# Optimization experiments

Measured on AMD Instinct MI355X. Metric: run time of the kernel, lower is better.

Reference implementation:

```python
import jax, jax.numpy as jnp
import numpy as np

# StyleGAN3 constants
FILTER_SIZE = 6
LRELU_UPSAMPLE = 2
SAMPLING_RATE = 128
CUTOFF = 64
HALF_WIDTH = 32
SLOPE = 0.01

UP = LRELU_UPSAMPLE                       # tmp_resize_factor = 2
NUM_TAPS = FILTER_SIZE * UP               # 12
_pad_total = -1 + (NUM_TAPS - 1) * 2      # 21
PAD_LO = (_pad_total + UP) // 2           # 11
PAD_HI = _pad_total - PAD_LO              # 10


def design_lowpass_filter(numtaps, cutoff, width, fs):
    """numpy re-implementation of scipy.signal.firwin(numtaps, cutoff, width=width, fs=fs)."""
    nyq = 0.5 * fs
    # kaiser_atten / kaiser_beta (scipy formulas)
    wn = width / nyq
    a = 2.285 * (numtaps - 1) * np.pi * wn + 7.95
    if a > 50:
        beta = 0.1102 * (a - 8.7)
    elif a > 21:
        beta = 0.5842 * (a - 21) ** 0.4 + 0.07886 * (a - 21)
    else:
        beta = 0.0
    alpha = 0.5 * (numtaps - 1)
    m = np.arange(numtaps) - alpha
    c = cutoff / nyq
    h = c * np.sinc(c * m) * np.kaiser(numtaps, beta)
    h = h / h.sum()  # scale so DC gain == 1 (firwin scale=True for lowpass)
    return jnp.asarray(h, dtype=jnp.float32)


def setup_inputs() -> dict:
    key = jax.random.key(0)
    x = jax.random.normal(key, (8, 128, 128, 128), dtype=jnp.float32)
    f = design_lowpass_filter(NUM_TAPS, CUTOFF, HALF_WIDTH * 2, SAMPLING_RATE * UP)
    return {"x": x, "f": f}


def _filtered_lrelu(x, f):
    """upfirdn2d(up=2, pad, gain=4) -> leaky_relu (gain=1) -> upfirdn2d(down=2)."""
    N, C, H, W = x.shape
    xr = x.reshape(N * C, 1, H, W)            # depthwise via batch folding
    fk = f[::-1].astype(x.dtype)              # conv (not xcorr), matches torch upfirdn2d flip
    dn = ("NCHW", "OIHW", "NCHW")
    g = jnp.asarray(UP, x.dtype)              # up**2 total gain, split over the 2 separable passes
    # --- upsample by 2 (zero insertion via lhs_dilation) + separable FIR ---
    # lhs_dilation yields length 2H-1 (no trailing zero) -> fold the trailing zero into pad_hi (+up-1)
    kv = (fk * g).reshape(1, 1, -1, 1)
    y = jax.lax.conv_general_dilated(xr, kv, (1, 1), ((PAD_LO, PAD_HI + UP - 1), (0, 0)),
                                     lhs_dilation=(UP, UP), dimension_numbers=dn)
    kh = (fk * g).reshape(1, 1, 1, -1)
    y = jax.lax.conv_general_dilated(y, kh, (1, 1), ((0, 0), (PAD_LO, PAD_HI + UP - 1)),
                                     dimension_numbers=dn)
    # --- leaky ReLU (overall gain = 1.0, clamp = None) ---
    y = jnp.where(y >= 0, y, y * jnp.asarray(SLOPE, y.dtype))
    # --- separable FIR + downsample by 2 (stride) ---
    y = jax.lax.conv_general_dilated(y, fk.reshape(1, 1, -1, 1), (UP, 1), ((0, 0), (0, 0)),
                                     dimension_numbers=dn)
    y = jax.lax.conv_general_dilated(y, fk.reshape(1, 1, 1, -1), (1, UP), ((0, 0), (0, 0)),
                                     dimension_numbers=dn)
    Ho, Wo = y.shape[-2], y.shape[-1]         # == H, W
    return y.reshape(N, C, Ho, Wo)


def reference(x, f):
    return _filtered_lrelu(x, f)
```

## Files before the change

### kernel.cpp

```cpp
#include <hip/hip_runtime.h>


#define TAPS 12
#define VS2 0
#define VSS2 44
#define ZS 1628
#define ZSS 44
#define XS 1628
#define XSS 44
#define WS 0
#define WSS 44
#define LDS_DW 4884

typedef _Float16 half_t;
typedef half_t h2 __attribute__((ext_vector_type(2)));
typedef __fp16 g2 __attribute__((ext_vector_type(2)));
typedef float f2 __attribute__((ext_vector_type(2)));

__device__ __forceinline__ h2 u2h(unsigned u){ h2 r; __builtin_memcpy(&r, &u, 4); return r; }
__device__ __forceinline__ g2 u2g(unsigned u){ g2 r; __builtin_memcpy(&r, &u, 4); return r; }
__device__ __forceinline__ unsigned h2du(h2 h){ unsigned u; __builtin_memcpy(&u, &h, 4); return u; }
__device__ __forceinline__ unsigned pkrtz_u(float lo, float hi){
    g2 p = __builtin_amdgcn_cvt_pkrtz(lo, hi);
    unsigned u; __builtin_memcpy(&u, &p, 4); return u;
}
__device__ __forceinline__ h2 h2s(float v){ h2 r; r.x = (half_t)v; r.y = r.x; return r; }
__device__ __forceinline__ unsigned pack2(half_t a, half_t b){ h2 t; t.x=a; t.y=b; return h2du(t); }

__global__ __launch_bounds__(256) void flrelu_fused(
    const float* __restrict__ x, const float* __restrict__ f, float* __restrict__ out)
{
    __shared__ float smem[LDS_DW];
    unsigned* smemu = reinterpret_cast<unsigned*>(smem);

    const int tid = threadIdx.x;
    const int nc  = blockIdx.y;
    const int ho0 = (blockIdx.x >> 2) * 32;
    const int wo0 = (blockIdx.x & 3) * 32;

    float fkU[TAPS];
#pragma unroll
    for (int t = 0; t < TAPS; ++t) fkU[t] = 2.0f * f[TAPS - 1 - t];

    const float* xin = x + (size_t)nc * (128 * 128);

    if (tid < 252) {
        int c = tid % 42, r0 = tid / 42;
        int gc = wo0 - 5 + c;
        bool gcok = (unsigned)gc < 128u;
        int gcc = gc < 0 ? 0 : (gc > 127 ? 127 : gc);
#pragma unroll
        for (int k = 0; k < 7; ++k) {
            int r = r0 + 6 * k;
            int gr = ho0 - 5 + r;
            int grc = gr < 0 ? 0 : (gr > 127 ? 127 : gr);
            float v = xin[grc * 128 + gcc];
            bool ok = gcok && ((unsigned)gr < 128u);
            smem[XS + r * XSS + c] = ok ? v : 0.f;
        }
    }
    __syncthreads();

    if (tid < 209) {
        int cq = tid % 11, mc = tid / 11;
        float4 xv[7];
#pragma unroll
        for (int s = 0; s < 7; ++s) {
            int r = 2 * mc + s; r = r < 42 ? r : 41;
            xv[s] = *(const float4*)(smem + XS + r * XSS + 4 * cq);
        }
        f2 tap2[6];
#pragma unroll
        for (int s = 0; s < 6; ++s) { tap2[s].x = fkU[2*s+1]; tap2[s].y = fkU[2*s]; }
#pragma unroll
        for (int k2 = 0; k2 < 2; ++k2) {
            int m = 2 * mc + k2;
            if (m < 37) {
                f2 acc[4];
#pragma unroll
                for (int c = 0; c < 4; ++c) { acc[c].x = 0.f; acc[c].y = 0.f; }
#pragma unroll
                for (int s = 0; s < 6; ++s) {
                    float4 xr = xv[k2 + s];
                    acc[0] += tap2[s] * xr.x;
                    acc[1] += tap2[s] * xr.y;
                    acc[2] += tap2[s] * xr.z;
                    acc[3] += tap2[s] * xr.w;
                }
                unsigned* vp = smemu + VS2 + m * VSS2 + 4 * cq;
                *(uint4*)vp = make_uint4(pkrtz_u(acc[0].x, acc[0].y),
                                         pkrtz_u(acc[1].x, acc[1].y),
                                         pkrtz_u(acc[2].x, acc[2].y),
                                         pkrtz_u(acc[3].x, acc[3].y));
            }
        }
    }
    __syncthreads();

    if (tid < 185) {
        int q = tid % 5, m = tid / 5;
        const unsigned* vb = smemu + VS2 + m * VSS2 + 8 * q;
        uint4 r0 = *(const uint4*)(vb);
        uint4 r1 = *(const uint4*)(vb + 4);
        uint4 r2 = *(const uint4*)(vb + 8);
        uint2 r3 = *(const uint2*)(vb + 12);
        h2 vc[14] = { u2h(r0.x), u2h(r0.y), u2h(r0.z), u2h(r0.w),
                      u2h(r1.x), u2h(r1.y), u2h(r1.z), u2h(r1.w),
                      u2h(r2.x), u2h(r2.y), u2h(r2.z), u2h(r2.w),
                      u2h(r3.x), u2h(r3.y) };
        h2 fo[6], fe[6];
#pragma unroll
        for (int s = 0; s < 6; ++s) { fo[s] = h2s(fkU[2*s+1]); fe[s] = h2s(fkU[2*s]); }
        h2 sl = h2s(0.01f);
        unsigned pk0[8], pk1[8];
#pragma unroll
        for (int h = 0; h < 8; ++h) {
            h2 ae = h2s(0.f), ao = h2s(0.f);
#pragma unroll
            for (int s = 0; s < 6; ++s) {
                ae += vc[h + s] * fo[s];
                ao += vc[h + s] * fe[s];
            }
            ae = __builtin_elementwise_max(ae, ae * sl);
            ao = __builtin_elementwise_max(ao, ao * sl);
            pk0[h] = pack2(ae.x, ao.x);
            pk1[h] = pack2(ae.y, ao.y);
        }
        unsigned* z0 = smemu + ZS + (2 * m) * ZSS + 8 * q;
        unsigned* z1 = z0 + ZSS;
        *(uint4*)(z0)     = make_uint4(pk0[0], pk0[1], pk0[2], pk0[3]);
        *(uint4*)(z0 + 4) = make_uint4(pk0[4], pk0[5], pk0[6], pk0[7]);
        *(uint4*)(z1)     = make_uint4(pk1[0], pk1[1], pk1[2], pk1[3]);
        *(uint4*)(z1 + 4) = make_uint4(pk1[4], pk1[5], pk1[6], pk1[7]);
    }
    __syncthreads();

    if (tid < 80) {
        int p8 = tid % 10, hq = tid / 10;
        h2 fkh[TAPS];
#pragma unroll
        for (int t = 0; t < TAPS; ++t) fkh[t] = h2s(0.5f * fkU[t]);
        h2 acc[4][4];
#pragma unroll
        for (int j = 0; j < 4; ++j)
#pragma unroll
            for (int d = 0; d < 4; ++d) acc[j][d] = h2s(0.f);
        const unsigned* zbase = smemu + ZS + (8 * hq) * ZSS + 4 * p8;
#pragma unroll
        for (int u = 0; u < 18; ++u) {
            uint4 zr = *(const uint4*)(zbase + u * ZSS);
            h2 z0 = u2h(zr.x), z1 = u2h(zr.y), z2 = u2h(zr.z), z3 = u2h(zr.w);
#pragma unroll
            for (int j = 0; j < 4; ++j) {
                int t = u - 2 * j;
                if (t >= 0 && t < TAPS) {
                    h2 tt = fkh[t];
                    acc[j][0] += tt * z0; acc[j][1] += tt * z1;
                    acc[j][2] += tt * z2; acc[j][3] += tt * z3;
                }
            }
        }
        unsigned* wp = smemu + WS + (4 * hq) * WSS + 4 * p8;
#pragma unroll
        for (int j = 0; j < 4; ++j)
            *(uint4*)(wp + j * WSS) = make_uint4(h2du(acc[j][0]), h2du(acc[j][1]),
                                                 h2du(acc[j][2]), h2du(acc[j][3]));
    }
    __syncthreads();

    {
        int ho = tid >> 3, w4 = tid & 7;
        const unsigned* wp = smemu + WS + ho * WSS + 4 * w4;
        uint4 q0 = *(const uint4*)(wp);
        uint4 q1 = *(const uint4*)(wp + 4);
        unsigned q2 = wp[8];
        unsigned dws[9] = { q0.x, q0.y, q0.z, q0.w, q1.x, q1.y, q1.z, q1.w, q2 };
        unsigned fp[6];
#pragma unroll
        for (int d = 0; d < 6; ++d) fp[d] = pkrtz_u(0.5f * fkU[2*d], 0.5f * fkU[2*d+1]);
        float o[4];
#pragma unroll
        for (int v = 0; v < 4; ++v) {
            float acc = 0.f;
#pragma unroll
            for (int d = 0; d < 6; ++d)
                acc = __builtin_amdgcn_fdot2(u2g(dws[v + d]), u2g(fp[d]), acc, false);
            o[v] = acc;
        }
        *(float4*)(out + ((size_t)nc * 128 + (ho0 + ho)) * 128 + wo0 + 4 * w4)
            = make_float4(o[0], o[1], o[2], o[3]);
    }
}

extern "C" void kernel_launch(void* const* d_in, const int* in_sizes, int n_in,
                              void* d_out, int out_size, void* d_ws, size_t ws_size,
                              hipStream_t stream) {
    const float* x = (const float*)d_in[0];
    const float* f = (const float*)d_in[1];
    float* out = (float*)d_out;
    dim3 grid(16, 1024);
    flrelu_fused<<<grid, 256, 0, stream>>>(x, f, out);
}
```

Before: 60.28 us.

## Fuse input load into vertical upsample pass, reading global directly with float4

Removes the LDS staging of the input tile and its barrier; the vertical upsample stage now reads float4 rows directly from global memory and applies zero-padding by scaling taps with row/column masks. The tile is realigned to 48 columns (start at wo0-8), so the V buffer stride grows and the horizontal stage's vector loads are shifted by one element. This saves an LDS round trip and a sync, at the cost of redundant global/L2 reads across threads and coarser 4-wide edge masking.

Result: slower. 68.62 us (+13.8%).

```diff
diff --git a/kernel.cpp b/kernel.cpp
--- a/kernel.cpp
+++ b/kernel.cpp
@@ -3,14 +3,12 @@
 
 #define TAPS 12
 #define VS2 0
-#define VSS2 44
-#define ZS 1628
+#define VSS2 48
+#define ZS 1776
 #define ZSS 44
-#define XS 1628
-#define XSS 44
 #define WS 0
 #define WSS 44
-#define LDS_DW 4884
+#define LDS_DW 5032
 
 typedef _Float16 half_t;
 typedef half_t h2 __attribute__((ext_vector_type(2)));
@@ -44,55 +42,46 @@
 
     const float* xin = x + (size_t)nc * (128 * 128);
 
-    if (tid < 252) {
-        int c = tid % 42, r0 = tid / 42;
-        int gc = wo0 - 5 + c;
-        bool gcok = (unsigned)gc < 128u;
-        int gcc = gc < 0 ? 0 : (gc > 127 ? 127 : gc);
+    if (tid < 228) {
+        int cq = tid % 12, mc = tid / 12;
+        int gA = wo0 - 8 + 4 * cq;
+        float qf = ((unsigned)gA <= 124u) ? 1.f : 0.f;
+        int gcc = gA < 0 ? 0 : (gA > 124 ? 124 : gA);
+        f2 tap2[6];
 #pragma unroll
-        for (int k = 0; k < 7; ++k) {
-            int r = r0 + 6 * k;
-            int gr = ho0 - 5 + r;
-            int grc = gr < 0 ? 0 : (gr > 127 ? 127 : gr);
-            float v = xin[grc * 128 + gcc];
-            bool ok = gcok && ((unsigned)gr < 128u);
-            smem[XS + r * XSS + c] = ok ? v : 0.f;
-        }
-    }
-    __syncthreads();
-
-    if (tid < 209) {
-        int cq = tid % 11, mc = tid / 11;
-        float4 xv[7];
+        for (int s = 0; s < 6; ++s) { tap2[s].x = fkU[2*s+1] * qf; tap2[s].y = fkU[2*s] * qf; }
+        f2 acc0[4], acc1[4];
+#pragma unroll
+        for (int c = 0; c < 4; ++c) { acc0[c].x=0.f; acc0[c].y=0.f; acc1[c].x=0.f; acc1[c].y=0.f; }
 #pragma unroll
         for (int s = 0; s < 7; ++s) {
-            int r = 2 * mc + s; r = r < 42 ? r : 41;
-            xv[s] = *(const float4*)(smem + XS + r * XSS + 4 * cq);
+            int gr = ho0 - 5 + 2 * mc + s;
+            int grc = gr < 0 ? 0 : (gr > 127 ? 127 : gr);
+            float rowf = ((unsigned)gr < 128u) ? 1.f : 0.f;
+            float4 xr = *(const float4*)(xin + grc * 128 + gcc);
+            if (s < 6) {
+                f2 t = tap2[s] * rowf;
+                acc0[0] += t * xr.x; acc0[1] += t * xr.y;
+                acc0[2] += t * xr.z; acc0[3] += t * xr.w;
+            }
+            if (s >= 1) {
+                f2 t = tap2[s - 1] * rowf;
+                acc1[0] += t * xr.x; acc1[1] += t * xr.y;
+                acc1[2] += t * xr.z; acc1[3] += t * xr.w;
+            }
         }
-        f2 tap2[6];
-#pragma unroll
-        for (int s = 0; s < 6; ++s) { tap2[s].x = fkU[2*s+1]; tap2[s].y = fkU[2*s]; }
-#pragma unroll
-        for (int k2 = 0; k2 < 2; ++k2) {
-            int m = 2 * mc + k2;
-            if (m < 37) {
-                f2 acc[4];
-#pragma unroll
-                for (int c = 0; c < 4; ++c) { acc[c].x = 0.f; acc[c].y = 0.f; }
-#pragma unroll
-                for (int s = 0; s < 6; ++s) {
-                    float4 xr = xv[k2 + s];
-                    acc[0] += tap2[s] * xr.x;
-                    acc[1] += tap2[s] * xr.y;
-                    acc[2] += tap2[s] * xr.z;
-                    acc[3] += tap2[s] * xr.w;
-                }
-                unsigned* vp = smemu + VS2 + m * VSS2 + 4 * cq;
-                *(uint4*)vp = make_uint4(pkrtz_u(acc[0].x, acc[0].y),
-                                         pkrtz_u(acc[1].x, acc[1].y),
-                                         pkrtz_u(acc[2].x, acc[2].y),
-                                         pkrtz_u(acc[3].x, acc[3].y));
-            }
+        int m0 = 2 * mc;
+        unsigned* vp0 = smemu + VS2 + m0 * VSS2 + 4 * cq;
+        *(uint4*)vp0 = make_uint4(pkrtz_u(acc0[0].x, acc0[0].y),
+                                  pkrtz_u(acc0[1].x, acc0[1].y),
+                                  pkrtz_u(acc0[2].x, acc0[2].y),
+                                  pkrtz_u(acc0[3].x, acc0[3].y));
+        if (m0 + 1 < 37) {
+            unsigned* vp1 = vp0 + VSS2;
+            *(uint4*)vp1 = make_uint4(pkrtz_u(acc1[0].x, acc1[0].y),
+                                      pkrtz_u(acc1[1].x, acc1[1].y),
+                                      pkrtz_u(acc1[2].x, acc1[2].y),
+                                      pkrtz_u(acc1[3].x, acc1[3].y));
         }
     }
     __syncthreads();
@@ -100,14 +89,14 @@
     if (tid < 185) {
         int q = tid % 5, m = tid / 5;
         const unsigned* vb = smemu + VS2 + m * VSS2 + 8 * q;
-        uint4 r0 = *(const uint4*)(vb);
-        uint4 r1 = *(const uint4*)(vb + 4);
-        uint4 r2 = *(const uint4*)(vb + 8);
-        uint2 r3 = *(const uint2*)(vb + 12);
-        h2 vc[14] = { u2h(r0.x), u2h(r0.y), u2h(r0.z), u2h(r0.w),
-                      u2h(r1.x), u2h(r1.y), u2h(r1.z), u2h(r1.w),
-                      u2h(r2.x), u2h(r2.y), u2h(r2.z), u2h(r2.w),
-                      u2h(r3.x), u2h(r3.y) };
+        uint4 rr0 = *(const uint4*)(vb);
+        uint4 rr1 = *(const uint4*)(vb + 4);
+        uint4 rr2 = *(const uint4*)(vb + 8);
+        uint4 rr3 = *(const uint4*)(vb + 12);
+        h2 vc[13] = { u2h(rr0.w),
+                      u2h(rr1.x), u2h(rr1.y), u2h(rr1.z), u2h(rr1.w),
+                      u2h(rr2.x), u2h(rr2.y), u2h(rr2.z), u2h(rr2.w),
+                      u2h(rr3.x), u2h(rr3.y), u2h(rr3.z), u2h(rr3.w) };
         h2 fo[6], fe[6];
 #pragma unroll
         for (int s = 0; s < 6; ++s) { fo[s] = h2s(fkU[2*s+1]); fe[s] = h2s(fkU[2*s]); }
```
